# Kernel tuning notes

Hardware: AMD Instinct MI355X
Metric: run time of the kernel (lower is better)

Reference implementation:

```python
import jax, jax.numpy as jnp
import numpy as np

B, T, D = 2, 2048, 1024
H, RANK = 16, 32
DH = D // H  # 64


def setup_inputs() -> dict:
    key = jax.random.key(0)
    ks = jax.random.split(key, 6)
    sd = 1.0 / np.sqrt(D)
    sdh = 1.0 / np.sqrt(DH)
    return {
        "x": jax.random.normal(ks[0], (B, T, D), dtype=jnp.float32),
        "W_qkv": jax.random.normal(ks[1], (D, 3 * D), dtype=jnp.float32) * sd,
        "W_q_lsr": jax.random.normal(ks[2], (H, DH, RANK), dtype=jnp.float32) * sdh,
        "W_k_lsr": jax.random.normal(ks[3], (H, DH, RANK), dtype=jnp.float32) * sdh,
        "lsr_core": jnp.ones((H, RANK), dtype=jnp.float32),
        "W_o": jax.random.normal(ks[4], (D, D), dtype=jnp.float32) * sd,
    }


def reference(x, W_qkv, W_q_lsr, W_k_lsr, lsr_core, W_o):
    b, t, d = x.shape
    # Fused QKV projection
    qkv = x @ W_qkv  # (B, T, 3D)
    q, k, v = jnp.split(qkv, 3, axis=-1)
    # (B, H, T, DH)
    q = q.reshape(b, t, H, DH).transpose(0, 2, 1, 3)
    k = k.reshape(b, t, H, DH).transpose(0, 2, 1, 3)
    v = v.reshape(b, t, H, DH).transpose(0, 2, 1, 3)
    # Low-rank bilinear score: q^T Wq diag(core) Wk^T k
    ql = jnp.einsum("bhtd,hdr->bhtr", q, W_q_lsr)  # (B, H, T, R)
    kl = jnp.einsum("bhsd,hdr->bhsr", k, W_k_lsr)  # (B, H, T, R)
    scale = 1.0 / jnp.sqrt(jnp.asarray(RANK, dtype=x.dtype))
    scores = jnp.einsum("bhtr,bhsr->bhts", ql * lsr_core[None, :, None, :], kl) * scale
    # Causal mask
    causal = jnp.tril(jnp.ones((t, t), dtype=bool))
    scores = jnp.where(causal[None, None], scores, jnp.asarray(-jnp.inf, dtype=scores.dtype))
    attn = jax.nn.softmax(scores, axis=-1)
    y = jnp.einsum("bhts,bhsd->bhtd", attn, v)  # (B, H, T, DH)
    y = y.transpose(0, 2, 1, 3).reshape(b, t, d)
    return y @ W_o
```

## Files before the change

kernel.cpp:

```cpp
#include <hip/hip_runtime.h>
#include <hip/hip_bf16.h>

#define B_  2
#define T_  2048
#define D_  1024
#define H_  16
#define DH_ 64
#define R_  32
#define BT_ (B_*T_)
#define BH_ (B_*H_)

typedef unsigned short u16;
typedef unsigned int   u32;
typedef __attribute__((ext_vector_type(8))) short bhalf8;
typedef __attribute__((ext_vector_type(4))) float floatx4;

#define WSB_FLAG  0
#define WSB_XB    256
#define WSB_WCATT (WSB_XB    + 8388608)
#define WSB_QL    (WSB_WCATT + 4194304)
#define WSB_KL    (WSB_QL    + 4194304)
#define WSB_VT    (WSB_KL    + 4194304)
#define WSB_YB    (WSB_VT    + 8388608)
#define WSB_WOT   (WSB_YB    + 8388608)

#define NEG_ -1.0e30f

__device__ __forceinline__ float bfs(u16 s) {
    union { u32 i; float f; } w; w.i = ((u32)s) << 16; return w.f;
}
__device__ __forceinline__ u16 tob(float f) {
    __hip_bfloat16 h = __float2bfloat16(f);
    return *(u16*)&h;
}
__device__ __forceinline__ u32 pack2(float a, float b) {
    return (u32)tob(a) | ((u32)tob(b) << 16);
}

__global__ __launch_bounds__(64) void detect_dtype(const u32* __restrict__ xw,
                                                   int* __restrict__ flag)
{
    const int tid = threadIdx.x;
    int hits = 0;
    for (int i = tid; i < 512; i += 64) {
        const u32 w = xw[i];
        const u32 h = w & 0xFFFFu;
        const u32 e = (h >> 7) & 0xFFu;
        if (h == 0u || (e >= 100u && e <= 150u)) ++hits;
    }
    #pragma unroll
    for (int off = 32; off; off >>= 1) hits += __shfl_down(hits, off, 64);
    if (tid == 0) *flag = (hits >= 300) ? 1 : 0;
}

__global__ __launch_bounds__(256) void convert_x(
    const void* __restrict__ x, u16* __restrict__ xb,
    const int* __restrict__ flag)
{
    const int isbf = *flag;
    const int e = blockIdx.x * 256 + threadIdx.x;
    if (isbf) {
        ((uint4*)xb)[e] = ((const uint4*)x)[e];
    } else {
        float4 a0 = ((const float4*)x)[2*e];
        float4 a1 = ((const float4*)x)[2*e + 1];
        uint4 o;
        o.x = pack2(a0.x, a0.y); o.y = pack2(a0.z, a0.w);
        o.z = pack2(a1.x, a1.y); o.w = pack2(a1.z, a1.w);
        ((uint4*)xb)[e] = o;
    }
}

__global__ __launch_bounds__(256) void fold_mfma(
    const void* __restrict__ Wqkv, const void* __restrict__ Wq_lsr,
    const void* __restrict__ Wk_lsr, const void* __restrict__ core,
    u16* __restrict__ WcatT, const int* __restrict__ flag)
{
    __shared__ __align__(16) u16 Bq[128 * 72];
    __shared__ __align__(16) u16 Bk[128 * 72];
    __shared__ __align__(16) u16 Aq[32 * 72];
    __shared__ __align__(16) u16 Ak[32 * 72];
    const int isbf = *flag;
    const int tid  = threadIdx.x;
    const int lane = tid & 63;
    const int w    = tid >> 6;
    const int n16  = lane & 15;
    const int q4   = lane >> 4;
    const int h    = blockIdx.y;
    const int d0   = blockIdx.x * 128;

    #pragma unroll
    for (int p = 0; p < 8; ++p) {
        const int e  = tid + p * 256;
        const int r  = e & 31, dh = e >> 5;
        float aq, ak;
        if (isbf) {
            aq = bfs(((const u16*)Wq_lsr)[(h*DH_ + dh)*R_ + r]);
            ak = bfs(((const u16*)Wk_lsr)[(h*DH_ + dh)*R_ + r]);
        } else {
            aq = ((const float*)Wq_lsr)[(h*DH_ + dh)*R_ + r];
            ak = ((const float*)Wk_lsr)[(h*DH_ + dh)*R_ + r];
        }
        Aq[r * 72 + dh] = tob(aq);
        Ak[r * 72 + dh] = tob(ak);
    }
    #pragma unroll
    for (int p = 0; p < 8; ++p) {
        const int e  = tid + p * 256;
        const int n  = e >> 4, ch = e & 15;
        if (isbf) {
            uint2 wq = *(const uint2*)((const u16*)Wqkv + (size_t)(d0+n)*(3*D_) + h*DH_ + ch*4);
            uint2 wk = *(const uint2*)((const u16*)Wqkv + (size_t)(d0+n)*(3*D_) + D_ + h*DH_ + ch*4);
            *(uint2*)&Bq[n * 72 + ch*4] = wq;
            *(uint2*)&Bk[n * 72 + ch*4] = wk;
        } else {
            float4 fq = *(const float4*)((const float*)Wqkv + (size_t)(d0+n)*(3*D_) + h*DH_ + ch*4);
            float4 fk = *(const float4*)((const float*)Wqkv + (size_t)(d0+n)*(3*D_) + D_ + h*DH_ + ch*4);
            uint2 oq, ok;
            oq.x = pack2(fq.x, fq.y); oq.y = pack2(fq.z, fq.w);
            ok.x = pack2(fk.x, fk.y); ok.y = pack2(fk.z, fk.w);
            *(uint2*)&Bq[n * 72 + ch*4] = oq;
            *(uint2*)&Bk[n * 72 + ch*4] = ok;
        }
    }
    __syncthreads();

    floatx4 accq[2][2], acck[2][2];
    #pragma unroll
    for (int mi = 0; mi < 2; ++mi)
        #pragma unroll
        for (int ni = 0; ni < 2; ++ni) { accq[mi][ni] = (floatx4)(0.f); acck[mi][ni] = (floatx4)(0.f); }

    #pragma unroll
    for (int kk = 0; kk < 2; ++kk) {
        bhalf8 aqf[2], akf[2], bqf[2], bkf[2];
        #pragma unroll
        for (int mi = 0; mi < 2; ++mi) {
            aqf[mi] = *(const bhalf8*)&Aq[(mi*16 + n16) * 72 + kk*32 + q4*8];
            akf[mi] = *(const bhalf8*)&Ak[(mi*16 + n16) * 72 + kk*32 + q4*8];
        }
        #pragma unroll
        for (int ni = 0; ni < 2; ++ni) {
            bqf[ni] = *(const bhalf8*)&Bq[(w*32 + ni*16 + n16) * 72 + kk*32 + q4*8];
            bkf[ni] = *(const bhalf8*)&Bk[(w*32 + ni*16 + n16) * 72 + kk*32 + q4*8];
        }
        #pragma unroll
        for (int mi = 0; mi < 2; ++mi)
            #pragma unroll
            for (int ni = 0; ni < 2; ++ni) {
                accq[mi][ni] = __builtin_amdgcn_mfma_f32_16x16x32_bf16(aqf[mi], bqf[ni], accq[mi][ni], 0, 0, 0);
                acck[mi][ni] = __builtin_amdgcn_mfma_f32_16x16x32_bf16(akf[mi], bkf[ni], acck[mi][ni], 0, 0, 0);
            }
    }

    const float scale = (float)(0.17677669529663687 * 1.4426950408889634);
    #pragma unroll
    for (int mi = 0; mi < 2; ++mi) {
        #pragma unroll
        for (int rr = 0; rr < 4; ++rr) {
            const int r = mi*16 + q4*4 + rr;
            const float cc = (isbf ? bfs(((const u16*)core)[h*R_ + r])
                                   : ((const float*)core)[h*R_ + r]) * scale;
            #pragma unroll
            for (int ni = 0; ni < 2; ++ni) {
                const int d = d0 + w*32 + ni*16 + n16;
                WcatT[(size_t)(h*R_ + r) * D_ + d]       = tob(accq[mi][ni][rr] * cc);
                WcatT[(size_t)(512 + h*R_ + r) * D_ + d] = tob(acck[mi][ni][rr]);
            }
        }
    }
}

__global__ __launch_bounds__(256) void convert_T(
    const void* __restrict__ src, u16* __restrict__ dst,
    int srcStride, int srcColOff, int dstRowOff, const int* __restrict__ flag)
{
    __shared__ __align__(16) u16 tile[64 * 72];
    const int isbf = *flag;
    const int tid = threadIdx.x;
    const int j0  = blockIdx.x * 64;
    const int i0  = blockIdx.y * 64;
    #pragma unroll
    for (int p = 0; p < 2; ++p) {
        const int e = tid + p * 256;
        const int r = e >> 3, ch = e & 7;
        if (isbf) {
            uint4 w = *(const uint4*)((const u16*)src + (size_t)(i0 + r) * srcStride + srcColOff + j0 + ch*8);
            *(uint4*)&tile[r * 72 + ch*8] = w;
        } else {
            const float* s = (const float*)src + (size_t)(i0 + r) * srcStride + srcColOff + j0 + ch*8;
            float4 a0 = *(const float4*)s;
            float4 a1 = *(const float4*)(s + 4);
            uint4 o;
            o.x = pack2(a0.x, a0.y); o.y = pack2(a0.z, a0.w);
            o.z = pack2(a1.x, a1.y); o.w = pack2(a1.z, a1.w);
            *(uint4*)&tile[r * 72 + ch*8] = o;
        }
    }
    __syncthreads();
    #pragma unroll
    for (int p = 0; p < 2; ++p) {
        const int e = tid + p * 256;
        const int c = e >> 3, ch = e & 7;
        u16 tmp[8];
        #pragma unroll
        for (int j = 0; j < 8; ++j) tmp[j] = tile[(ch*8 + j) * 72 + c];
        *(uint4*)(dst + (size_t)(dstRowOff + j0 + c) * D_ + i0 + ch*8) = *(uint4*)tmp;
    }
}

__global__ __launch_bounds__(256) void gemm1_mfma(
    const u16* __restrict__ xb, const u16* __restrict__ WcatT,
    u16* __restrict__ ql, u16* __restrict__ kl, u16* __restrict__ v_t)
{
    __shared__ __align__(16) u16 As[128 * 72];
    __shared__ __align__(16) u16 Bs[64 * 72];
    const int tid  = threadIdx.x;
    const int lane = tid & 63;
    const int w    = tid >> 6;
    const int n16  = lane & 15;
    const int q4   = lane >> 4;
    const int wx   = w & 1;
    const int wy   = w >> 1;
    const int bm   = blockIdx.y * 128;
    const int bn   = blockIdx.x * 64;

    floatx4 acc[4][2];
    #pragma unroll
    for (int i = 0; i < 4; ++i)
        #pragma unroll
        for (int j = 0; j < 2; ++j) acc[i][j] = (floatx4)(0.f);

    for (int kt = 0; kt < D_; kt += 64) {
        #pragma unroll
        for (int p = 0; p < 4; ++p) {
            const int e = tid + p * 256;
            const int r = e >> 3, ch = (e & 7) * 8;
            *(uint4*)&As[r * 72 + ch] = *(const uint4*)(xb + (size_t)(bm + r) * D_ + kt + ch);
        }
        #pragma unroll
        for (int p = 0; p < 2; ++p) {
            const int e = tid + p * 256;
            const int r = e >> 3, ch = (e & 7) * 8;
            *(uint4*)&Bs[r * 72 + ch] = *(const uint4*)(WcatT + (size_t)(bn + r) * D_ + kt + ch);
        }
        __syncthreads();
        #pragma unroll
        for (int kk = 0; kk < 2; ++kk) {
            bhalf8 a[4], b[2];
            #pragma unroll
            for (int mi = 0; mi < 4; ++mi)
                a[mi] = *(const bhalf8*)&As[(wy*64 + mi*16 + n16) * 72 + kk*32 + q4*8];
            #pragma unroll
            for (int ni = 0; ni < 2; ++ni)
                b[ni] = *(const bhalf8*)&Bs[(wx*32 + ni*16 + n16) * 72 + kk*32 + q4*8];
            #pragma unroll
            for (int mi = 0; mi < 4; ++mi)
                #pragma unroll
                for (int ni = 0; ni < 2; ++ni)
                    acc[mi][ni] = __builtin_amdgcn_mfma_f32_16x16x32_bf16(
                        a[mi], b[ni], acc[mi][ni], 0, 0, 0);
        }
        __syncthreads();
    }

    if (bn < 1024) {
        #pragma unroll
        for (int mi = 0; mi < 4; ++mi) {
            #pragma unroll
            for (int rr = 0; rr < 4; ++rr) {
                const int row = bm + wy*64 + mi*16 + q4*4 + rr;
                const int b   = row >> 11;
                const int t   = row & (T_ - 1);
                #pragma unroll
                for (int ni = 0; ni < 2; ++ni) {
                    const int col = bn + wx*32 + ni*16 + n16;
                    const u16 val = tob(acc[mi][ni][rr]);
                    if (col < 512) {
                        const int h = col >> 5, r = col & 31;
                        ql[((size_t)(b*H_ + h)*T_ + t)*R_ + r] = val;
                    } else {
                        const int c = col - 512; const int h = c >> 5, r = c & 31;
                        kl[((size_t)(b*H_ + h)*T_ + t)*R_ + r] = val;
                    }
                }
            }
        }
    } else {
        #pragma unroll
        for (int mi = 0; mi < 4; ++mi) {
            const int row0 = bm + wy*64 + mi*16 + q4*4;
            const int b = row0 >> 11;
            const int t = row0 & (T_ - 1);
            #pragma unroll
            for (int ni = 0; ni < 2; ++ni) {
                const int c = bn - 1024 + wx*32 + ni*16 + n16;
                const int h = c >> 6, dh = c & 63;
                uint2 o;
                o.x = pack2(acc[mi][ni][0], acc[mi][ni][1]);
                o.y = pack2(acc[mi][ni][2], acc[mi][ni][3]);
                *(uint2*)(v_t + ((size_t)(b*H_ + h) * DH_ + dh) * T_ + t) = o;
            }
        }
    }
}

__global__ __launch_bounds__(256, 4) void attn_kernel(
    const u16* __restrict__ ql, const u16* __restrict__ kl,
    const u16* __restrict__ v_t, u16* __restrict__ y)
{
    __shared__ __align__(16) u16 kls[128 * 40];
    __shared__ __align__(16) u16 vsT[64 * 136];

    const int tid  = threadIdx.x;
    const int lane = tid & 63;
    const int w    = tid >> 6;
    const int n16  = lane & 15;
    const int q4   = lane >> 4;
    const int bh   = blockIdx.x;
    const int qt   = 31 - (int)blockIdx.y;
    const int t0   = qt * 64;
    const int nt   = (qt + 2) >> 1;

    const u16* qlb = ql + (size_t)bh * T_ * R_;
    const bhalf8 aq = *(const bhalf8*)(qlb + (size_t)(t0 + w*16 + n16) * R_ + q4*8);

    const u16* klb = kl  + (size_t)bh * T_ * R_;
    const u16* vtb = v_t + (size_t)bh * DH_ * T_;
    const int rk = tid >> 2, ck = (tid & 3) * 8;
    const int dv = tid >> 4;
    const int m  = tid & 15;
    const int cv = m * 8;
    const int pb = ((m & 1) << 4) | (((m >> 1) & 1) << 2) | ((m >> 2) << 5);

    uint4 kc0 = *(const uint4*)(klb + (size_t)(rk     ) * R_ + ck);
    uint4 kc1 = *(const uint4*)(klb + (size_t)(rk + 64) * R_ + ck);
    uint4 vc0 = *(const uint4*)(vtb + (size_t)(dv     ) * T_ + cv);
    uint4 vc1 = *(const uint4*)(vtb + (size_t)(dv + 16) * T_ + cv);
    uint4 vc2 = *(const uint4*)(vtb + (size_t)(dv + 32) * T_ + cv);
    uint4 vc3 = *(const uint4*)(vtb + (size_t)(dv + 48) * T_ + cv);
    uint4 kn0 = kc0, kn1 = kc1, vn0 = vc0, vn1 = vc1, vn2 = vc2, vn3 = vc3;

    float mrow = NEG_, lrow = 0.f;
    floatx4 O[4];
    #pragma unroll
    for (int c = 0; c < 4; ++c) O[c] = (floatx4)(0.f);

    for (int it = 0; it < nt; ++it) {
        const int s0 = it * 128;
        __syncthreads();
        *(uint4*)&kls[(rk     ) * 40 + ck] = kc0;
        *(uint4*)&kls[(rk + 64) * 40 + ck] = kc1;
        {
            uint2 t;
            t.x = vc0.x; t.y = vc0.y; *(uint2*)&vsT[(dv     ) * 136 + pb    ] = t;
            t.x = vc0.z; t.y = vc0.w; *(uint2*)&vsT[(dv     ) * 136 + pb + 8] = t;
            t.x = vc1.x; t.y = vc1.y; *(uint2*)&vsT[(dv + 16) * 136 + pb    ] = t;
            t.x = vc1.z; t.y = vc1.w; *(uint2*)&vsT[(dv + 16) * 136 + pb + 8] = t;
            t.x = vc2.x; t.y = vc2.y; *(uint2*)&vsT[(dv + 32) * 136 + pb    ] = t;
            t.x = vc2.z; t.y = vc2.w; *(uint2*)&vsT[(dv + 32) * 136 + pb + 8] = t;
            t.x = vc3.x; t.y = vc3.y; *(uint2*)&vsT[(dv + 48) * 136 + pb    ] = t;
            t.x = vc3.z; t.y = vc3.w; *(uint2*)&vsT[(dv + 48) * 136 + pb + 8] = t;
        }
        if (it + 1 < nt) {
            const int s1 = s0 + 128;
            kn0 = *(const uint4*)(klb + (size_t)(s1 + rk     ) * R_ + ck);
            kn1 = *(const uint4*)(klb + (size_t)(s1 + rk + 64) * R_ + ck);
            vn0 = *(const uint4*)(vtb + (size_t)(dv     ) * T_ + s1 + cv);
            vn1 = *(const uint4*)(vtb + (size_t)(dv + 16) * T_ + s1 + cv);
            vn2 = *(const uint4*)(vtb + (size_t)(dv + 32) * T_ + s1 + cv);
            vn3 = *(const uint4*)(vtb + (size_t)(dv + 48) * T_ + s1 + cv);
        }
        __syncthreads();

        floatx4 Sc[8];
        #pragma unroll
        for (int c = 0; c < 8; ++c) {
            bhalf8 ak = *(const bhalf8*)&kls[(16*c + n16) * 40 + q4*8];
            Sc[c] = __builtin_amdgcn_mfma_f32_16x16x32_bf16(ak, aq, (floatx4)(0.f), 0, 0, 0);
        }

        if (it == nt - 1) {
            const int tq = w*16 + n16;
            #pragma unroll
            for (int c = 0; c < 8; ++c) {
                const int sb = s0 - t0 + 16*c + 4*q4;
                #pragma unroll
                for (int r = 0; r < 4; ++r)
                    if (sb + r > tq) Sc[c][r] = NEG_;
            }
        }

        float cmax[8];
        #pragma unroll
        for (int c = 0; c < 8; ++c)
            cmax[c] = fmaxf(fmaxf(Sc[c][0], Sc[c][1]), fmaxf(Sc[c][2], Sc[c][3]));
        float rmax = fmaxf(fmaxf(fmaxf(cmax[0], cmax[1]), fmaxf(cmax[2], cmax[3])),
                           fmaxf(fmaxf(cmax[4], cmax[5]), fmaxf(cmax[6], cmax[7])));
        rmax = fmaxf(rmax, __shfl_xor(rmax, 16, 64));
        rmax = fmaxf(rmax, __shfl_xor(rmax, 32, 64));

        const float mn = fmaxf(mrow, rmax);
        const int norescale = __all(rmax <= mrow);

        float csum[8];
        #pragma unroll
        for (int c = 0; c < 8; ++c) {
            #pragma unroll
            for (int r = 0; r < 4; ++r)
                Sc[c][r] = __builtin_amdgcn_exp2f(Sc[c][r] - mn);
            csum[c] = (Sc[c][0] + Sc[c][1]) + (Sc[c][2] + Sc[c][3]);
        }
        float rsum = ((csum[0] + csum[1]) + (csum[2] + csum[3]))
                   + ((csum[4] + csum[5]) + (csum[6] + csum[7]));
        rsum += __shfl_xor(rsum, 16, 64);
        rsum += __shfl_xor(rsum, 32, 64);

        if (norescale) {
            lrow += rsum;
        } else {
            const float alpha = __builtin_amdgcn_exp2f(mrow - mn);
            mrow = mn;
            lrow = lrow * alpha + rsum;
            float aO[4];
            #pragma unroll
            for (int r = 0; r < 4; ++r) aO[r] = __shfl(alpha, q4*4 + r, 64);
            #pragma unroll
            for (int c2 = 0; c2 < 4; ++c2)
                #pragma unroll
                for (int r = 0; r < 4; ++r) O[c2][r] *= aO[r];
        }

        #pragma unroll
        for (int kc = 0; kc < 4; ++kc) {
            union { u32 wd[4]; bhalf8 v; } pu;
            pu.wd[0] = pack2(Sc[2*kc    ][0], Sc[2*kc    ][1]);
            pu.wd[1] = pack2(Sc[2*kc    ][2], Sc[2*kc    ][3]);
            pu.wd[2] = pack2(Sc[2*kc + 1][0], Sc[2*kc + 1][1]);
            pu.wd[3] = pack2(Sc[2*kc + 1][2], Sc[2*kc + 1][3]);
            const bhalf8 pa = pu.v;
            #pragma unroll
            for (int c2 = 0; c2 < 4; ++c2) {
                bhalf8 bv = *(const bhalf8*)&vsT[(16*c2 + n16) * 136 + kc*32 + q4*8];
                O[c2] = __builtin_amdgcn_mfma_f32_16x16x32_bf16(pa, bv, O[c2], 0, 0, 0);
            }
        }

        kc0 = kn0; kc1 = kn1; vc0 = vn0; vc1 = vn1; vc2 = vn2; vc3 = vn3;
    }

    const int b = bh >> 4, h = bh & 15;
    float lb[4];
    #pragma unroll
    for (int r = 0; r < 4; ++r) lb[r] = __shfl(lrow, q4*4 + r, 64);
    #pragma unroll
    for (int r = 0; r < 4; ++r) {
        const float rl = 1.0f / lb[r];
        const int t = t0 + w*16 + q4*4 + r;
        #pragma unroll
        for (int c2 = 0; c2 < 4; ++c2)
            y[((size_t)b * T_ + t) * D_ + h * DH_ + 16*c2 + n16] = tob(O[c2][r] * rl);
    }
}

__global__ __launch_bounds__(256) void out_gemm_mfma(
    const u16* __restrict__ yb, const u16* __restrict__ WoT,
    float* __restrict__ out)
{
    __shared__ __align__(16) u16 As[128 * 72];
    __shared__ __align__(16) u16 Bs[64 * 72];
    const int tid  = threadIdx.x;
    const int lane = tid & 63;
    const int w    = tid >> 6;
    const int n16  = lane & 15;
    const int q4   = lane >> 4;
    const int wx   = w & 1;
    const int wy   = w >> 1;
    const int bm   = blockIdx.y * 128;
    const int bn   = blockIdx.x * 64;

    floatx4 acc[4][2];
    #pragma unroll
    for (int i = 0; i < 4; ++i)
        #pragma unroll
        for (int j = 0; j < 2; ++j) acc[i][j] = (floatx4)(0.f);

    for (int kt = 0; kt < D_; kt += 64) {
        #pragma unroll
        for (int p = 0; p < 4; ++p) {
            const int e = tid + p * 256;
            const int r = e >> 3, ch = (e & 7) * 8;
            *(uint4*)&As[r * 72 + ch] = *(const uint4*)(yb + (size_t)(bm + r) * D_ + kt + ch);
        }
        #pragma unroll
        for (int p = 0; p < 2; ++p) {
            const int e = tid + p * 256;
            const int r = e >> 3, ch = (e & 7) * 8;
            *(uint4*)&Bs[r * 72 + ch] = *(const uint4*)(WoT + (size_t)(bn + r) * D_ + kt + ch);
        }
        __syncthreads();
        #pragma unroll
        for (int kk = 0; kk < 2; ++kk) {
            bhalf8 a[4], b[2];
            #pragma unroll
            for (int mi = 0; mi < 4; ++mi)
                a[mi] = *(const bhalf8*)&As[(wy*64 + mi*16 + n16) * 72 + kk*32 + q4*8];
            #pragma unroll
            for (int ni = 0; ni < 2; ++ni)
                b[ni] = *(const bhalf8*)&Bs[(wx*32 + ni*16 + n16) * 72 + kk*32 + q4*8];
            #pragma unroll
            for (int mi = 0; mi < 4; ++mi)
                #pragma unroll
                for (int ni = 0; ni < 2; ++ni)
                    acc[mi][ni] = __builtin_amdgcn_mfma_f32_16x16x32_bf16(
                        a[mi], b[ni], acc[mi][ni], 0, 0, 0);
        }
        __syncthreads();
    }

    #pragma unroll
    for (int mi = 0; mi < 4; ++mi) {
        #pragma unroll
        for (int rr = 0; rr < 4; ++rr) {
            const int row = bm + wy*64 + mi*16 + q4*4 + rr;
            #pragma unroll
            for (int ni = 0; ni < 2; ++ni) {
                const int col = bn + wx*32 + ni*16 + n16;
                out[(size_t)row * D_ + col] = acc[mi][ni][rr];
            }
        }
    }
}

extern "C" void kernel_launch(void* const* d_in, const int* in_sizes, int n_in,
                              void* d_out, int out_size, void* d_ws, size_t ws_size,
                              hipStream_t stream)
{
    (void)out_size; (void)ws_size;
    const void* in_x = nullptr; const void* in_wqkv = nullptr;
    const void* in_wq = nullptr; const void* in_wk = nullptr;
    const void* in_core = nullptr; const void* in_wo = nullptr;
    for (int i = 0; i < n_in; ++i) {
        const int s = in_sizes[i];
        if      (s == BT_*D_)     { if (!in_x)    in_x    = d_in[i]; }
        else if (s == D_*3*D_)    { if (!in_wqkv) in_wqkv = d_in[i]; }
        else if (s == H_*DH_*R_)  { if (!in_wq)   in_wq   = d_in[i]; else if (!in_wk) in_wk = d_in[i]; }
        else if (s == H_*R_)      { if (!in_core) in_core = d_in[i]; }
        else if (s == D_*D_)      { if (!in_wo)   in_wo   = d_in[i]; }
    }
    if (!in_x)    in_x    = d_in[0];
    if (!in_wqkv) in_wqkv = d_in[1];
    if (!in_wq)   in_wq   = d_in[2];
    if (!in_wk)   in_wk   = d_in[3];
    if (!in_core) in_core = d_in[4];
    if (!in_wo)   in_wo   = d_in[5];

    float* out = (float*)d_out;

    char* ws    = (char*)d_ws;
    int*  flag  = (int*)(ws + WSB_FLAG);
    u16*  xb    = (u16*)(ws + WSB_XB);
    u16*  WcatT = (u16*)(ws + WSB_WCATT);
    u16*  ql    = (u16*)(ws + WSB_QL);
    u16*  kl    = (u16*)(ws + WSB_KL);
    u16*  v_t   = (u16*)(ws + WSB_VT);
    u16*  yb    = (u16*)(ws + WSB_YB);
    u16*  WoT   = (u16*)(ws + WSB_WOT);

    detect_dtype<<<1, 64, 0, stream>>>((const u32*)in_x, flag);
    convert_x<<<2048, 256, 0, stream>>>(in_x, xb, flag);
    fold_mfma<<<dim3(8, 16), 256, 0, stream>>>(in_wqkv, in_wq, in_wk, in_core, WcatT, flag);
    convert_T<<<dim3(16,16), 256, 0, stream>>>(in_wqkv, WcatT, 3*D_, 2*D_, 1024, flag);
    convert_T<<<dim3(16,16), 256, 0, stream>>>(in_wo,   WoT,   D_,   0,    0,    flag);
    gemm1_mfma<<<dim3(32, 32), 256, 0, stream>>>(xb, WcatT, ql, kl, v_t);
    attn_kernel<<<dim3(32, 32), 256, 0, stream>>>(ql, kl, v_t, yb);
    out_gemm_mfma<<<dim3(16, 32), 256, 0, stream>>>(yb, WoT, out);
}
```

Baseline: 189.5 us.

## Enlarge QKV GEMM tile to 128x128 and attention query tile to 128 rows

The first GEMM now computes 128x128 output tiles per block, each wave holding a 4x4 MFMA accumulator set, which halves the grid and reuses each loaded A tile across twice as many columns. The attention kernel now uses 512-thread blocks covering 128 query rows, so each K/V tile staged in shared memory serves eight waves instead of four, halving global K/V traffic per query. The query-tile order is also changed to pair long and short causal tiles, and the softmax is moved into a helper. The larger tiles raise register and shared-memory pressure and halve the block count, which may reduce occupancy or load balance.

```diff
diff --git a/kernel.cpp b/kernel.cpp
--- a/kernel.cpp
+++ b/kernel.cpp
@@ -209,9 +209,254 @@
     }
 }
 
-__global__ __launch_bounds__(256) void gemm1_mfma(
+__global__ __launch_bounds__(256, 2) void gemm1_mfma(
     const u16* __restrict__ xb, const u16* __restrict__ WcatT,
     u16* __restrict__ ql, u16* __restrict__ kl, u16* __restrict__ v_t)
+{
+    __shared__ __align__(16) u16 As[128 * 72];
+    __shared__ __align__(16) u16 Bs[128 * 72];
+    const int tid  = threadIdx.x;
+    const int lane = tid & 63;
+    const int w    = tid >> 6;
+    const int n16  = lane & 15;
+    const int q4   = lane >> 4;
+    const int wx   = w & 1;
+    const int wy   = w >> 1;
+    const int bm   = blockIdx.y * 128;
+    const int bn   = blockIdx.x * 128;
+
+    floatx4 acc[4][4];
+    #pragma unroll
+    for (int i = 0; i < 4; ++i)
+        #pragma unroll
+        for (int j = 0; j < 4; ++j) acc[i][j] = (floatx4)(0.f);
+
+    for (int kt = 0; kt < D_; kt += 64) {
+        #pragma unroll
+        for (int p = 0; p < 4; ++p) {
+            const int e = tid + p * 256;
+            const int r = e >> 3, ch = (e & 7) * 8;
+            *(uint4*)&As[r * 72 + ch] = *(const uint4*)(xb    + (size_t)(bm + r) * D_ + kt + ch);
+            *(uint4*)&Bs[r * 72 + ch] = *(const uint4*)(WcatT + (size_t)(bn + r) * D_ + kt + ch);
+        }
+        __syncthreads();
+        #pragma unroll
+        for (int kk = 0; kk < 2; ++kk) {
+            bhalf8 a[4], b[4];
+            #pragma unroll
+            for (int mi = 0; mi < 4; ++mi)
+                a[mi] = *(const bhalf8*)&As[(wy*64 + mi*16 + n16) * 72 + kk*32 + q4*8];
+            #pragma unroll
+            for (int ni = 0; ni < 4; ++ni)
+                b[ni] = *(const bhalf8*)&Bs[(wx*64 + ni*16 + n16) * 72 + kk*32 + q4*8];
+            #pragma unroll
+            for (int mi = 0; mi < 4; ++mi)
+                #pragma unroll
+                for (int ni = 0; ni < 4; ++ni)
+                    acc[mi][ni] = __builtin_amdgcn_mfma_f32_16x16x32_bf16(
+                        a[mi], b[ni], acc[mi][ni], 0, 0, 0);
+        }
+        __syncthreads();
+    }
+
+    if (bn < 1024) {
+        #pragma unroll
+        for (int mi = 0; mi < 4; ++mi) {
+            #pragma unroll
+            for (int rr = 0; rr < 4; ++rr) {
+                const int row = bm + wy*64 + mi*16 + q4*4 + rr;
+                const int b   = row >> 11;
+                const int t   = row & (T_ - 1);
+                #pragma unroll
+                for (int ni = 0; ni < 4; ++ni) {
+                    const int col = bn + wx*64 + ni*16 + n16;
+                    const u16 val = tob(acc[mi][ni][rr]);
+                    if (col < 512) {
+                        const int h = col >> 5, r = col & 31;
+                        ql[((size_t)(b*H_ + h)*T_ + t)*R_ + r] = val;
+                    } else {
+                        const int c = col - 512; const int h = c >> 5, r = c & 31;
+                        kl[((size_t)(b*H_ + h)*T_ + t)*R_ + r] = val;
+                    }
+                }
+            }
+        }
+    } else {
+        #pragma unroll
+        for (int mi = 0; mi < 4; ++mi) {
+            const int row0 = bm + wy*64 + mi*16 + q4*4;
+            const int b = row0 >> 11;
+            const int t = row0 & (T_ - 1);
+            #pragma unroll
+            for (int ni = 0; ni < 4; ++ni) {
+                const int c = bn - 1024 + wx*64 + ni*16 + n16;
+                const int h = c >> 6, dh = c & 63;
+                uint2 o;
+                o.x = pack2(acc[mi][ni][0], acc[mi][ni][1]);
+                o.y = pack2(acc[mi][ni][2], acc[mi][ni][3]);
+                *(uint2*)(v_t + ((size_t)(b*H_ + h) * DH_ + dh) * T_ + t) = o;
+            }
+        }
+    }
+}
+
+__device__ __forceinline__ void softmax_update(
+    floatx4 (&Sc)[8], float &mrow, float &lrow, floatx4 (&O)[4], int q4)
+{
+    float cmax[8];
+    #pragma unroll
+    for (int c = 0; c < 8; ++c)
+        cmax[c] = fmaxf(fmaxf(Sc[c][0], Sc[c][1]), fmaxf(Sc[c][2], Sc[c][3]));
+    float rmax = fmaxf(fmaxf(fmaxf(cmax[0], cmax[1]), fmaxf(cmax[2], cmax[3])),
+                       fmaxf(fmaxf(cmax[4], cmax[5]), fmaxf(cmax[6], cmax[7])));
+    rmax = fmaxf(rmax, __shfl_xor(rmax, 16, 64));
+    rmax = fmaxf(rmax, __shfl_xor(rmax, 32, 64));
+
+    const float mn = fmaxf(mrow, rmax);
+    const int norescale = __all(rmax <= mrow);
+
+    float csum[8];
+    #pragma unroll
+    for (int c = 0; c < 8; ++c) {
+        #pragma unroll
+        for (int r = 0; r < 4; ++r)
+            Sc[c][r] = __builtin_amdgcn_exp2f(Sc[c][r] - mn);
+        csum[c] = (Sc[c][0] + Sc[c][1]) + (Sc[c][2] + Sc[c][3]);
+    }
+    float rsum = ((csum[0] + csum[1]) + (csum[2] + csum[3]))
+               + ((csum[4] + csum[5]) + (csum[6] + csum[7]));
+    rsum += __shfl_xor(rsum, 16, 64);
+    rsum += __shfl_xor(rsum, 32, 64);
+
+    if (norescale) {
+        lrow += rsum;
+    } else {
+        const float alpha = __builtin_amdgcn_exp2f(mrow - mn);
+        mrow = mn;
+        lrow = lrow * alpha + rsum;
+        float aO[4];
+        #pragma unroll
+        for (int r = 0; r < 4; ++r) aO[r] = __shfl(alpha, q4*4 + r, 64);
+        #pragma unroll
+        for (int c2 = 0; c2 < 4; ++c2)
+            #pragma unroll
+            for (int r = 0; r < 4; ++r) O[c2][r] *= aO[r];
+    }
+}
+
+__global__ __launch_bounds__(512, 4) void attn_kernel(
+    const u16* __restrict__ ql, const u16* __restrict__ kl,
+    const u16* __restrict__ v_t, u16* __restrict__ y)
+{
+    __shared__ __align__(16) u16 kls[128 * 40];
+    __shared__ __align__(16) u16 vsT[64 * 136];
+
+    const int tid  = threadIdx.x;
+    const int lane = tid & 63;
+    const int w    = tid >> 6;
+    const int n16  = lane & 15;
+    const int q4   = lane >> 4;
+    const int bh   = blockIdx.x;
+    const int by   = blockIdx.y;
+    const int qt2  = (by < 8) ? (15 - by) : (by - 8);
+    const int t0   = qt2 * 128;
+    const int nt   = qt2 + 1;
+
+    const u16* qlb = ql + (size_t)bh * T_ * R_;
+    const bhalf8 aq = *(const bhalf8*)(qlb + (size_t)(t0 + w*16 + n16) * R_ + q4*8);
+
+    const u16* klb = kl  + (size_t)bh * T_ * R_;
+    const u16* vtb = v_t + (size_t)bh * DH_ * T_;
+    const int rk = tid >> 2, ck = (tid & 3) * 8;
+    const int dv = tid >> 4;
+    const int m  = tid & 15;
+    const int cv = m * 8;
+    const int pb = ((m & 1) << 4) | (((m >> 1) & 1) << 2) | ((m >> 2) << 5);
+
+    uint4 kc0 = *(const uint4*)(klb + (size_t)(rk     ) * R_ + ck);
+    uint4 vc0 = *(const uint4*)(vtb + (size_t)(dv     ) * T_ + cv);
+    uint4 vc1 = *(const uint4*)(vtb + (size_t)(dv + 32) * T_ + cv);
+    uint4 kn0 = kc0, vn0 = vc0, vn1 = vc1;
+
+    float mrow = NEG_, lrow = 0.f;
+    floatx4 O[4];
+    #pragma unroll
+    for (int c = 0; c < 4; ++c) O[c] = (floatx4)(0.f);
+
+    for (int it = 0; it < nt; ++it) {
+        const int s0 = it * 128;
+        __syncthreads();
+        *(uint4*)&kls[rk * 40 + ck] = kc0;
+        {
+            uint2 t;
+            t.x = vc0.x; t.y = vc0.y; *(uint2*)&vsT[(dv     ) * 136 + pb    ] = t;
+            t.x = vc0.z; t.y = vc0.w; *(uint2*)&vsT[(dv     ) * 136 + pb + 8] = t;
+            t.x = vc1.x; t.y = vc1.y; *(uint2*)&vsT[(dv + 32) * 136 + pb    ] = t;
+            t.x = vc1.z; t.y = vc1.w; *(uint2*)&vsT[(dv + 32) * 136 + pb + 8] = t;
+        }
+        if (it + 1 < nt) {
+            const int s1 = s0 + 128;
+            kn0 = *(const uint4*)(klb + (size_t)(s1 + rk) * R_ + ck);
+            vn0 = *(const uint4*)(vtb + (size_t)(dv     ) * T_ + s1 + cv);
+            vn1 = *(const uint4*)(vtb + (size_t)(dv + 32) * T_ + s1 + cv);
+        }
+        __syncthreads();
+
+        floatx4 Sc[8];
+        #pragma unroll
+        for (int c = 0; c < 8; ++c) {
+            bhalf8 ak = *(const bhalf8*)&kls[(16*c + n16) * 40 + q4*8];
+            Sc[c] = __builtin_amdgcn_mfma_f32_16x16x32_bf16(ak, aq, (floatx4)(0.f), 0, 0, 0);
+        }
+
+        if (it == nt - 1) {
+            const int tq = w*16 + n16;
+            #pragma unroll
+            for (int c = 0; c < 8; ++c) {
+                const int sb = 16*c + 4*q4;
+                #pragma unroll
+                for (int r = 0; r < 4; ++r)
+                    if (sb + r > tq) Sc[c][r] = NEG_;
+            }
+        }
+
+        softmax_update(Sc, mrow, lrow, O, q4);
+
+        #pragma unroll
+        for (int kc = 0; kc < 4; ++kc) {
+            union { u32 wd[4]; bhalf8 v; } pu;
+            pu.wd[0] = pack2(Sc[2*kc    ][0], Sc[2*kc    ][1]);
+            pu.wd[1] = pack2(Sc[2*kc    ][2], Sc[2*kc    ][3]);
+            pu.wd[2] = pack2(Sc[2*kc + 1][0], Sc[2*kc + 1][1]);
+            pu.wd[3] = pack2(Sc[2*kc + 1][2], Sc[2*kc + 1][3]);
+            const bhalf8 pa = pu.v;
+            #pragma unroll
+            for (int c2 = 0; c2 < 4; ++c2) {
+                bhalf8 bv = *(const bhalf8*)&vsT[(16*c2 + n16) * 136 + kc*32 + q4*8];
+                O[c2] = __builtin_amdgcn_mfma_f32_16x16x32_bf16(pa, bv, O[c2], 0, 0, 0);
+            }
+        }
+
+        kc0 = kn0; vc0 = vn0; vc1 = vn1;
+    }
+
+    const int b = bh >> 4, h = bh & 15;
+    float lb[4];
+    #pragma unroll
+    for (int r = 0; r < 4; ++r) lb[r] = __shfl(lrow, q4*4 + r, 64);
+    #pragma unroll
+    for (int r = 0; r < 4; ++r) {
+        const float rl = 1.0f / lb[r];
+        const int t = t0 + w*16 + q4*4 + r;
+        #pragma unroll
+        for (int c2 = 0; c2 < 4; ++c2)
+            y[((size_t)b * T_ + t) * D_ + h * DH_ + 16*c2 + n16] = tob(O[c2][r] * rl);
+    }
+}
+
+__global__ __launch_bounds__(256) void out_gemm_mfma(
+    const u16* __restrict__ yb, const u16* __restrict__ WoT,
+    float* __restrict__ out)
 {
     __shared__ __align__(16) u16 As[128 * 72];
     __shared__ __align__(16) u16 Bs[64 * 72];
@@ -236,260 +481,6 @@
         for (int p = 0; p < 4; ++p) {
             const int e = tid + p * 256;
             const int r = e >> 3, ch = (e & 7) * 8;
-            *(uint4*)&As[r * 72 + ch] = *(const uint4*)(xb + (size_t)(bm + r) * D_ + kt + ch);
-        }
-        #pragma unroll
-        for (int p = 0; p < 2; ++p) {
-            const int e = tid + p * 256;
-            const int r = e >> 3, ch = (e & 7) * 8;
-            *(uint4*)&Bs[r * 72 + ch] = *(const uint4*)(WcatT + (size_t)(bn + r) * D_ + kt + ch);
-        }
-        __syncthreads();
-        #pragma unroll
-        for (int kk = 0; kk < 2; ++kk) {
-            bhalf8 a[4], b[2];
-            #pragma unroll
-            for (int mi = 0; mi < 4; ++mi)
-                a[mi] = *(const bhalf8*)&As[(wy*64 + mi*16 + n16) * 72 + kk*32 + q4*8];
-            #pragma unroll
-            for (int ni = 0; ni < 2; ++ni)
-                b[ni] = *(const bhalf8*)&Bs[(wx*32 + ni*16 + n16) * 72 + kk*32 + q4*8];
-            #pragma unroll
-            for (int mi = 0; mi < 4; ++mi)
-                #pragma unroll
-                for (int ni = 0; ni < 2; ++ni)
-                    acc[mi][ni] = __builtin_amdgcn_mfma_f32_16x16x32_bf16(
-                        a[mi], b[ni], acc[mi][ni], 0, 0, 0);
-        }
-        __syncthreads();
-    }
-
-    if (bn < 1024) {
-        #pragma unroll
-        for (int mi = 0; mi < 4; ++mi) {
-            #pragma unroll
-            for (int rr = 0; rr < 4; ++rr) {
-                const int row = bm + wy*64 + mi*16 + q4*4 + rr;
-                const int b   = row >> 11;
-                const int t   = row & (T_ - 1);
-                #pragma unroll
-                for (int ni = 0; ni < 2; ++ni) {
-                    const int col = bn + wx*32 + ni*16 + n16;
-                    const u16 val = tob(acc[mi][ni][rr]);
-                    if (col < 512) {
-                        const int h = col >> 5, r = col & 31;
-                        ql[((size_t)(b*H_ + h)*T_ + t)*R_ + r] = val;
-                    } else {
-                        const int c = col - 512; const int h = c >> 5, r = c & 31;
-                        kl[((size_t)(b*H_ + h)*T_ + t)*R_ + r] = val;
-                    }
-                }
-            }
-        }
-    } else {
-        #pragma unroll
-        for (int mi = 0; mi < 4; ++mi) {
-            const int row0 = bm + wy*64 + mi*16 + q4*4;
-            const int b = row0 >> 11;
-            const int t = row0 & (T_ - 1);
-            #pragma unroll
-            for (int ni = 0; ni < 2; ++ni) {
-                const int c = bn - 1024 + wx*32 + ni*16 + n16;
-                const int h = c >> 6, dh = c & 63;
-                uint2 o;
-                o.x = pack2(acc[mi][ni][0], acc[mi][ni][1]);
-                o.y = pack2(acc[mi][ni][2], acc[mi][ni][3]);
-                *(uint2*)(v_t + ((size_t)(b*H_ + h) * DH_ + dh) * T_ + t) = o;
-            }
-        }
-    }
-}
-
-__global__ __launch_bounds__(256, 4) void attn_kernel(
-    const u16* __restrict__ ql, const u16* __restrict__ kl,
-    const u16* __restrict__ v_t, u16* __restrict__ y)
-{
-    __shared__ __align__(16) u16 kls[128 * 40];
-    __shared__ __align__(16) u16 vsT[64 * 136];
-
-    const int tid  = threadIdx.x;
-    const int lane = tid & 63;
-    const int w    = tid >> 6;
-    const int n16  = lane & 15;
-    const int q4   = lane >> 4;
-    const int bh   = blockIdx.x;
-    const int qt   = 31 - (int)blockIdx.y;
-    const int t0   = qt * 64;
-    const int nt   = (qt + 2) >> 1;
-
-    const u16* qlb = ql + (size_t)bh * T_ * R_;
-    const bhalf8 aq = *(const bhalf8*)(qlb + (size_t)(t0 + w*16 + n16) * R_ + q4*8);
-
-    const u16* klb = kl  + (size_t)bh * T_ * R_;
-    const u16* vtb = v_t + (size_t)bh * DH_ * T_;
-    const int rk = tid >> 2, ck = (tid & 3) * 8;
-    const int dv = tid >> 4;
-    const int m  = tid & 15;
-    const int cv = m * 8;
-    const int pb = ((m & 1) << 4) | (((m >> 1) & 1) << 2) | ((m >> 2) << 5);
-
-    uint4 kc0 = *(const uint4*)(klb + (size_t)(rk     ) * R_ + ck);
-    uint4 kc1 = *(const uint4*)(klb + (size_t)(rk + 64) * R_ + ck);
-    uint4 vc0 = *(const uint4*)(vtb + (size_t)(dv     ) * T_ + cv);
-    uint4 vc1 = *(const uint4*)(vtb + (size_t)(dv + 16) * T_ + cv);
-    uint4 vc2 = *(const uint4*)(vtb + (size_t)(dv + 32) * T_ + cv);
-    uint4 vc3 = *(const uint4*)(vtb + (size_t)(dv + 48) * T_ + cv);
-    uint4 kn0 = kc0, kn1 = kc1, vn0 = vc0, vn1 = vc1, vn2 = vc2, vn3 = vc3;
-
-    float mrow = NEG_, lrow = 0.f;
-    floatx4 O[4];
-    #pragma unroll
-    for (int c = 0; c < 4; ++c) O[c] = (floatx4)(0.f);
-
-    for (int it = 0; it < nt; ++it) {
-        const int s0 = it * 128;
-        __syncthreads();
-        *(uint4*)&kls[(rk     ) * 40 + ck] = kc0;
-        *(uint4*)&kls[(rk + 64) * 40 + ck] = kc1;
-        {
-            uint2 t;
-            t.x = vc0.x; t.y = vc0.y; *(uint2*)&vsT[(dv     ) * 136 + pb    ] = t;
-            t.x = vc0.z; t.y = vc0.w; *(uint2*)&vsT[(dv     ) * 136 + pb + 8] = t;
-            t.x = vc1.x; t.y = vc1.y; *(uint2*)&vsT[(dv + 16) * 136 + pb    ] = t;
-            t.x = vc1.z; t.y = vc1.w; *(uint2*)&vsT[(dv + 16) * 136 + pb + 8] = t;
-            t.x = vc2.x; t.y = vc2.y; *(uint2*)&vsT[(dv + 32) * 136 + pb    ] = t;
-            t.x = vc2.z; t.y = vc2.w; *(uint2*)&vsT[(dv + 32) * 136 + pb + 8] = t;
-            t.x = vc3.x; t.y = vc3.y; *(uint2*)&vsT[(dv + 48) * 136 + pb    ] = t;
-            t.x = vc3.z; t.y = vc3.w; *(uint2*)&vsT[(dv + 48) * 136 + pb + 8] = t;
-        }
-        if (it + 1 < nt) {
-            const int s1 = s0 + 128;
-            kn0 = *(const uint4*)(klb + (size_t)(s1 + rk     ) * R_ + ck);
-            kn1 = *(const uint4*)(klb + (size_t)(s1 + rk + 64) * R_ + ck);
-            vn0 = *(const uint4*)(vtb + (size_t)(dv     ) * T_ + s1 + cv);
-            vn1 = *(const uint4*)(vtb + (size_t)(dv + 16) * T_ + s1 + cv);
-            vn2 = *(const uint4*)(vtb + (size_t)(dv + 32) * T_ + s1 + cv);
-            vn3 = *(const uint4*)(vtb + (size_t)(dv + 48) * T_ + s1 + cv);
-        }
-        __syncthreads();
-
-        floatx4 Sc[8];
-        #pragma unroll
-        for (int c = 0; c < 8; ++c) {
-            bhalf8 ak = *(const bhalf8*)&kls[(16*c + n16) * 40 + q4*8];
-            Sc[c] = __builtin_amdgcn_mfma_f32_16x16x32_bf16(ak, aq, (floatx4)(0.f), 0, 0, 0);
-        }
-
-        if (it == nt - 1) {
-            const int tq = w*16 + n16;
-            #pragma unroll
-            for (int c = 0; c < 8; ++c) {
-                const int sb = s0 - t0 + 16*c + 4*q4;
-                #pragma unroll
-                for (int r = 0; r < 4; ++r)
-                    if (sb + r > tq) Sc[c][r] = NEG_;
-            }
-        }
-
-        float cmax[8];
-        #pragma unroll
-        for (int c = 0; c < 8; ++c)
-            cmax[c] = fmaxf(fmaxf(Sc[c][0], Sc[c][1]), fmaxf(Sc[c][2], Sc[c][3]));
-        float rmax = fmaxf(fmaxf(fmaxf(cmax[0], cmax[1]), fmaxf(cmax[2], cmax[3])),
-                           fmaxf(fmaxf(cmax[4], cmax[5]), fmaxf(cmax[6], cmax[7])));
-        rmax = fmaxf(rmax, __shfl_xor(rmax, 16, 64));
-        rmax = fmaxf(rmax, __shfl_xor(rmax, 32, 64));
-
-        const float mn = fmaxf(mrow, rmax);
-        const int norescale = __all(rmax <= mrow);
-
-        float csum[8];
-        #pragma unroll
-        for (int c = 0; c < 8; ++c) {
-            #pragma unroll
-            for (int r = 0; r < 4; ++r)
-                Sc[c][r] = __builtin_amdgcn_exp2f(Sc[c][r] - mn);
-            csum[c] = (Sc[c][0] + Sc[c][1]) + (Sc[c][2] + Sc[c][3]);
-        }
-        float rsum = ((csum[0] + csum[1]) + (csum[2] + csum[3]))
-                   + ((csum[4] + csum[5]) + (csum[6] + csum[7]));
-        rsum += __shfl_xor(rsum, 16, 64);
-        rsum += __shfl_xor(rsum, 32, 64);
-
-        if (norescale) {
-            lrow += rsum;
-        } else {
-            const float alpha = __builtin_amdgcn_exp2f(mrow - mn);
-            mrow = mn;
-            lrow = lrow * alpha + rsum;
-            float aO[4];
-            #pragma unroll
-            for (int r = 0; r < 4; ++r) aO[r] = __shfl(alpha, q4*4 + r, 64);
-            #pragma unroll
-            for (int c2 = 0; c2 < 4; ++c2)
-                #pragma unroll
-                for (int r = 0; r < 4; ++r) O[c2][r] *= aO[r];
-        }
-
-        #pragma unroll
-        for (int kc = 0; kc < 4; ++kc) {
-            union { u32 wd[4]; bhalf8 v; } pu;
-            pu.wd[0] = pack2(Sc[2*kc    ][0], Sc[2*kc    ][1]);
-            pu.wd[1] = pack2(Sc[2*kc    ][2], Sc[2*kc    ][3]);
-            pu.wd[2] = pack2(Sc[2*kc + 1][0], Sc[2*kc + 1][1]);
-            pu.wd[3] = pack2(Sc[2*kc + 1][2], Sc[2*kc + 1][3]);
-            const bhalf8 pa = pu.v;
-            #pragma unroll
-            for (int c2 = 0; c2 < 4; ++c2) {
-                bhalf8 bv = *(const bhalf8*)&vsT[(16*c2 + n16) * 136 + kc*32 + q4*8];
-                O[c2] = __builtin_amdgcn_mfma_f32_16x16x32_bf16(pa, bv, O[c2], 0, 0, 0);
-            }
-        }
-
-        kc0 = kn0; kc1 = kn1; vc0 = vn0; vc1 = vn1; vc2 = vn2; vc3 = vn3;
-    }
-
-    const int b = bh >> 4, h = bh & 15;
-    float lb[4];
-    #pragma unroll
-    for (int r = 0; r < 4; ++r) lb[r] = __shfl(lrow, q4*4 + r, 64);
-    #pragma unroll
-    for (int r = 0; r < 4; ++r) {
-        const float rl = 1.0f / lb[r];
-        const int t = t0 + w*16 + q4*4 + r;
-        #pragma unroll
-        for (int c2 = 0; c2 < 4; ++c2)
-            y[((size_t)b * T_ + t) * D_ + h * DH_ + 16*c2 + n16] = tob(O[c2][r] * rl);
-    }
-}
-
-__global__ __launch_bounds__(256) void out_gemm_mfma(
-    const u16* __restrict__ yb, const u16* __restrict__ WoT,
-    float* __restrict__ out)
-{
-    __shared__ __align__(16) u16 As[128 * 72];
-    __shared__ __align__(16) u16 Bs[64 * 72];
-    const int tid  = threadIdx.x;
-    const int lane = tid & 63;
-    const int w    = tid >> 6;
-    const int n16  = lane & 15;
-    const int q4   = lane >> 4;
-    const int wx   = w & 1;
-    const int wy   = w >> 1;
-    const int bm   = blockIdx.y * 128;
-    const int bn   = blockIdx.x * 64;
-
-    floatx4 acc[4][2];
-    #pragma unroll
-    for (int i = 0; i < 4; ++i)
-        #pragma unroll
-        for (int j = 0; j < 2; ++j) acc[i][j] = (floatx4)(0.f);
-
-    for (int kt = 0; kt < D_; kt += 64) {
-        #pragma unroll
-        for (int p = 0; p < 4; ++p) {
-            const int e = tid + p * 256;
-            const int r = e >> 3, ch = (e & 7) * 8;
             *(uint4*)&As[r * 72 + ch] = *(const uint4*)(yb + (size_t)(bm + r) * D_ + kt + ch);
         }
         #pragma unroll
@@ -572,7 +563,7 @@
     fold_mfma<<<dim3(8, 16), 256, 0, stream>>>(in_wqkv, in_wq, in_wk, in_core, WcatT, flag);
     convert_T<<<dim3(16,16), 256, 0, stream>>>(in_wqkv, WcatT, 3*D_, 2*D_, 1024, flag);
     convert_T<<<dim3(16,16), 256, 0, stream>>>(in_wo,   WoT,   D_,   0,    0,    flag);
-    gemm1_mfma<<<dim3(32, 32), 256, 0, stream>>>(xb, WcatT, ql, kl, v_t);
-    attn_kernel<<<dim3(32, 32), 256, 0, stream>>>(ql, kl, v_t, yb);
+    gemm1_mfma<<<dim3(16, 32), 256, 0, stream>>>(xb, WcatT, ql, kl, v_t);
+    attn_kernel<<<dim3(32, 16), 512, 0, stream>>>(ql, kl, v_t, yb);
     out_gemm_mfma<<<dim3(16, 32), 256, 0, stream>>>(yb, WoT, out);
 }
```

Measured after the change: 185.4 us. 2.2% less time.
